# Kernel optimization log

Hardware: AMD Instinct MI355X
Metric: run time of the kernel (lower is better)

Reference implementation:

```python
import jax, jax.numpy as jnp
import numpy as np

V, T, E, HID = 50000, 32, 256, 512
H = HID // 2  # per-direction LSTM hidden
L, B = 512, 64


def setup_inputs() -> dict:
    key = jax.random.key(0)
    ks = jax.random.split(key, 18)
    p = lambda k, shape: (jax.random.normal(k, shape, jnp.float32) * 0.1)
    return {
        'seqs': jax.random.randint(ks[0], (L, B), 0, V),
        'tags': jax.random.randint(ks[1], (L, B), 0, T),
        'masks': jnp.ones((L, B), jnp.int32),
        'embed_table': p(ks[2], (V, E)),
        'W_ih_f': p(ks[3], (4 * H, E)), 'W_hh_f': p(ks[4], (4 * H, H)),
        'b_ih_f': p(ks[5], (4 * H,)),   'b_hh_f': p(ks[6], (4 * H,)),
        'W_ih_b': p(ks[7], (4 * H, E)), 'W_hh_b': p(ks[8], (4 * H, H)),
        'b_ih_b': p(ks[9], (4 * H,)),   'b_hh_b': p(ks[10], (4 * H,)),
        'W_out': p(ks[11], (T, HID)),   'b_out': p(ks[12], (T,)),
        'start_trans': p(ks[13], (T,)), 'end_trans': p(ks[14], (T,)),
        'trans': p(ks[15], (T, T)),
    }


def _lstm(xs, mask_b, W_ih, W_hh, b_ih, b_hh, reverse):
    # xs: [L,B,E], mask_b: [L,B] bool. Masked updates emulate packed sequences
    # (state frozen and output zeroed at padded steps).
    Bsz = xs.shape[1]
    Hd = W_hh.shape[1]
    x_proj = jnp.einsum('lbe,ge->lbg', xs, W_ih) + b_ih + b_hh  # precompute input gates

    def step(carry, inp):
        h, c = carry
        xg, m = inp
        gates = xg + h @ W_hh.T
        i, f, g, o = jnp.split(gates, 4, axis=-1)  # torch gate order i,f,g,o
        i, f, o = jax.nn.sigmoid(i), jax.nn.sigmoid(f), jax.nn.sigmoid(o)
        g = jnp.tanh(g)
        c_new = f * c + i * g
        h_new = o * jnp.tanh(c_new)
        m = m[:, None]
        h = jnp.where(m, h_new, h)
        c = jnp.where(m, c_new, c)
        out = jnp.where(m, h_new, 0.0)
        return (h, c), out

    init = (jnp.zeros((Bsz, Hd), xs.dtype), jnp.zeros((Bsz, Hd), xs.dtype))
    _, outs = jax.lax.scan(step, init, (x_proj, mask_b), reverse=reverse)
    return outs  # [L,B,H]


def reference(seqs, tags, masks, embed_table,
              W_ih_f, W_hh_f, b_ih_f, b_hh_f,
              W_ih_b, W_hh_b, b_ih_b, b_hh_b,
              W_out, b_out, start_trans, end_trans, trans):
    mb = masks.astype(bool)  # [L,B]
    emb = embed_table[seqs]  # [L,B,E]; dropout is identity in eval mode
    h_f = _lstm(emb, mb, W_ih_f, W_hh_f, b_ih_f, b_hh_f, reverse=False)
    h_b = _lstm(emb, mb, W_ih_b, W_hh_b, b_ih_b, b_hh_b, reverse=True)
    lstm_out = jnp.concatenate([h_f, h_b], axis=-1)           # [L,B,HID]
    emissions = jnp.einsum('lbh,th->lbt', lstm_out, W_out) + b_out  # [L,B,T]

    Lb, Bb = seqs.shape
    mf = masks[1:].astype(emissions.dtype)  # [L-1,B]

    # ---- gold path score (pytorch-crf numerator) ----
    e_scores = jnp.take_along_axis(emissions, tags[:, :, None], axis=2)[:, :, 0]  # [L,B]
    t_scores = trans[tags[:-1], tags[1:]]                                         # [L-1,B]
    lengths = masks.sum(0)
    last_tags = tags[lengths - 1, jnp.arange(Bb)]
    numerator = (start_trans[tags[0]] + e_scores[0]
                 + ((e_scores[1:] + t_scores) * mf).sum(0)
                 + end_trans[last_tags])  # [B]

    # ---- partition function (forward algorithm) ----
    def part_step(score, xs):
        e_t, m_t = xs  # [B,T], [B]
        nxt = jax.nn.logsumexp(score[:, :, None] + trans[None] + e_t[:, None, :], axis=1)
        return jnp.where(m_t[:, None], nxt, score), None

    score0 = start_trans[None, :] + emissions[0]
    score, _ = jax.lax.scan(part_step, score0, (emissions[1:], mb[1:]))
    log_z = jax.nn.logsumexp(score + end_trans[None, :], axis=1)  # [B]

    llh = numerator - log_z
    return -llh.mean()
```

## Files before the change

### kernel.cpp

```cpp
#include <hip/hip_runtime.h>
#include <hip/hip_bf16.h>
#include <stdint.h>

#define DEVINL __device__ __forceinline__

typedef __attribute__((ext_vector_type(8))) short short8;
typedef __attribute__((ext_vector_type(4))) float float4v;
typedef __attribute__((ext_vector_type(4))) int int4v;

#define NLC (-1.4426950408889634f)

DEVINL float uif(unsigned u) { union { unsigned u; float f; } v; v.u = u; return v.f; }
DEVINL float bf2f(short s) { return uif(((unsigned)(unsigned short)s) << 16); }
DEVINL unsigned short f2bf(float f) {
  union { float f; unsigned u; } v; v.f = f;
  unsigned r = v.u + 0x7FFFu + ((v.u >> 16) & 1u);
  return (unsigned short)(r >> 16);
}
DEVINL unsigned cvt_pk_bf16(float lo, float hi) {
  unsigned r;
  asm("v_cvt_pk_bf16_f32 %0, %1, %2" : "=v"(r) : "v"(lo), "v"(hi));
  return r;
}
DEVINL float ex2(float x) { return __builtin_amdgcn_exp2f(x); }
DEVINL float rcp_(float x) { return __builtin_amdgcn_rcpf(x); }
DEVINL void unp4(unsigned long long u, float* f) {
  unsigned lo = (unsigned)u, hi = (unsigned)(u >> 32);
  f[0] = uif(lo << 16); f[1] = uif(lo & 0xffff0000u);
  f[2] = uif(hi << 16); f[3] = uif(hi & 0xffff0000u);
}

#define LBAR() do { \
  asm volatile("s_waitcnt lgkmcnt(0)" ::: "memory"); \
  __builtin_amdgcn_sched_barrier(0); \
  __builtin_amdgcn_s_barrier(); \
  __builtin_amdgcn_sched_barrier(0); \
} while (0)

__global__ void k_cvt(const float* __restrict__ src, short* __restrict__ dst, int n8) {
  int i = blockIdx.x * blockDim.x + threadIdx.x;
  int stride = gridDim.x * blockDim.x;
  for (; i < n8; i += stride) {
    const float4v* s = (const float4v*)(src + (size_t)i * 8);
    float4v a = s[0], b = s[1];
    short8 o;
    o[0] = (short)f2bf(a[0]); o[1] = (short)f2bf(a[1]);
    o[2] = (short)f2bf(a[2]); o[3] = (short)f2bf(a[3]);
    o[4] = (short)f2bf(b[0]); o[5] = (short)f2bf(b[1]);
    o[6] = (short)f2bf(b[2]); o[7] = (short)f2bf(b[3]);
    ((short8*)dst)[i] = o;
  }
}

__global__ void k_bias(const float* __restrict__ a1, const float* __restrict__ a2,
                       const float* __restrict__ b1, const float* __restrict__ b2,
                       float* __restrict__ o) {
  int i = blockIdx.x * blockDim.x + threadIdx.x;
  o[i] = (i < 1024) ? (a1[i] + a2[i]) : (b1[i - 1024] + b2[i - 1024]);
}

__global__ void k_wmax(const float* __restrict__ Wf, const float* __restrict__ Wb,
                       unsigned* __restrict__ wmax) {
  int i = blockIdx.x * blockDim.x + threadIdx.x;
  int stride = gridDim.x * blockDim.x;
  unsigned mf = 0, mb = 0;
  for (int k = i; k < 262144; k += stride) {
    mf = max(mf, __float_as_uint(fabsf(Wf[k])));
    mb = max(mb, __float_as_uint(fabsf(Wb[k])));
  }
#pragma unroll
  for (int o = 32; o > 0; o >>= 1) {
    mf = max(mf, (unsigned)__shfl_down((int)mf, o));
    mb = max(mb, (unsigned)__shfl_down((int)mb, o));
  }
  if ((threadIdx.x & 63) == 0) { atomicMax(wmax + 0, mf); atomicMax(wmax + 1, mb); }
}

__global__ void k_wquant(const float* __restrict__ Wf, const float* __restrict__ Wb,
                         const float* __restrict__ wmax, char* __restrict__ whhQ) {
  int idx = blockIdx.x * blockDim.x + threadIdx.x;
  int dir = idx >> 16;
  int rem = idx & 65535;
  int r = rem >> 6;
  int k = (rem & 63) * 4;
  const float* W = dir ? Wb : Wf;
  float s = 127.0f / fmaxf(wmax[dir], 1e-20f);
  int g = r >> 8, unit = r & 255;
  int w = unit >> 6, m = (unit >> 4) & 3, row = unit & 15;
  int kt = k >> 6, l4 = (k >> 4) & 3, j = k & 15;
  int lane = l4 * 16 + row;
  unsigned out = 0;
#pragma unroll
  for (int t = 0; t < 4; ++t) {
    float v = W[(size_t)r * 256 + k + t] * s;
    int q = (int)rintf(v);
    q = q < -127 ? -127 : (q > 127 ? 127 : q);
    out |= ((unsigned)(q & 255)) << (8 * t);
  }
  *(unsigned*)(whhQ + (size_t)dir * 262144 + g * 65536 + w * 16384 + m * 4096 + kt * 1024 + lane * 16 + j) = out;
}

__launch_bounds__(256)
__global__ void k_xproj(const int* __restrict__ seqs, const short* __restrict__ embT,
                        const short* __restrict__ wihX, const float* __restrict__ biasX,
                        short* __restrict__ xproj) {
  __shared__ short As[128 * 256];
  __shared__ short Bs[128 * 256];
  __shared__ int ids[128];
  const int bm = blockIdx.x;
  const int tid = threadIdx.x;
  if (tid < 128) ids[tid] = seqs[bm * 128 + tid];
  __syncthreads();
#pragma unroll
  for (int i = 0; i < 16; ++i) {
    int task = tid + i * 256, row = task >> 5, kc = task & 31;
    short8 v = *(const short8*)(embT + (size_t)ids[row] * 256 + kc * 8);
    *(short8*)((char*)As + row * 512 + ((kc * 16) ^ ((row & 7) << 4))) = v;
  }
  __syncthreads();
  const int wave = tid >> 6, lane = tid & 63, l15 = lane & 15, l4 = lane >> 4;
  short8 af[2][8];
#pragma unroll
  for (int m = 0; m < 2; ++m) {
    int row = (wave * 2 + m) * 16 + l15;
#pragma unroll
    for (int kt = 0; kt < 8; ++kt)
      af[m][kt] = *(short8*)((char*)As + row * 512 + ((kt * 64 + l4 * 16) ^ ((row & 7) << 4)));
  }
#pragma unroll 1
  for (int bn = 0; bn < 16; ++bn) {
    __syncthreads();
#pragma unroll
    for (int i = 0; i < 16; ++i) {
      int task = tid + i * 256, row = task >> 5, kc = task & 31;
      short8 v = *(const short8*)(wihX + (size_t)(bn * 128 + row) * 256 + kc * 8);
      *(short8*)((char*)Bs + row * 512 + ((kc * 16) ^ ((row & 7) << 4))) = v;
    }
    __syncthreads();
    float4v acc[2][8];
#pragma unroll
    for (int m = 0; m < 2; ++m)
#pragma unroll
      for (int n = 0; n < 8; ++n) acc[m][n] = (float4v){0.f, 0.f, 0.f, 0.f};
#pragma unroll
    for (int kt = 0; kt < 8; ++kt) {
      const int kb = kt * 64 + l4 * 16;
      short8 b[8];
#pragma unroll
      for (int n = 0; n < 8; ++n) {
        int row = n * 16 + l15;
        b[n] = *(short8*)((char*)Bs + row * 512 + (kb ^ ((row & 7) << 4)));
      }
#pragma unroll
      for (int m = 0; m < 2; ++m)
#pragma unroll
        for (int n = 0; n < 8; ++n)
          acc[m][n] = __builtin_amdgcn_mfma_f32_16x16x32_bf16(af[m][kt], b[n], acc[m][n], 0, 0, 0);
    }
#pragma unroll
    for (int n = 0; n < 8; ++n) {
      int col = bn * 128 + n * 16 + l15;
      float bias = biasX[col];
      float scale = (((col >> 8) & 3) == 2) ? (2.f * NLC) : NLC;
#pragma unroll
      for (int m = 0; m < 2; ++m) {
        int token = bm * 128 + (wave * 2 + m) * 16 + l4 * 4;
#pragma unroll
        for (int q = 0; q < 4; ++q)
          xproj[(size_t)(token + q) * 2048 + col] = (short)f2bf((acc[m][n][q] + bias) * scale);
      }
    }
  }
}

__launch_bounds__(512, 2)
__global__ void k_lstm(const short* __restrict__ xproj, const char* __restrict__ whhQ,
                       const float* __restrict__ wmax, const int* __restrict__ mask_ws,
                       short* __restrict__ h_all) {
  __shared__ char lds_h[2][16 * 256];
  const int bid = blockIdx.x;
  const int dir = bid & 1, bq = bid >> 1;
  const int tid = threadIdx.x, w = tid >> 6, lane = tid & 63;
  const int beta = lane & 15, l4 = lane >> 4;
  const int bglob = bq * 16 + beta;
  const float wm = wmax[dir] * (1.0f / 16129.0f);
  const float facS = wm * NLC;
  const float facG = wm * 2.f * NLC;

  int4v wf[4][2][4];
  {
    const char* base = whhQ + (size_t)dir * 262144 + lane * 16;
#pragma unroll
    for (int g = 0; g < 4; ++g)
#pragma unroll
      for (int m = 0; m < 2; ++m) {
        int t = w * 2 + m;
#pragma unroll
        for (int kt = 0; kt < 4; ++kt)
          wf[g][m][kt] = *(const int4v*)(base + g * 65536 + (t >> 2) * 16384 + (t & 3) * 4096 + kt * 1024);
      }
  }

  int rd_off[4], wr_off[2];
#pragma unroll
  for (int kt = 0; kt < 4; ++kt)
    rd_off[kt] = beta * 256 + ((kt * 64 + l4 * 16) ^ ((beta & 7) << 4));
#pragma unroll
  for (int m = 0; m < 2; ++m)
    wr_off[m] = beta * 256 + ((w * 32 + m * 16 + l4 * 4) ^ ((beta & 7) << 4));

  if (tid < 256) ((int4v*)lds_h[0])[tid] = (int4v){0, 0, 0, 0};

  float c[2][4], hq[2][4];
#pragma unroll
  for (int m = 0; m < 2; ++m)
#pragma unroll
    for (int q = 0; q < 4; ++q) { c[m][q] = 0.f; hq[m][q] = 0.f; }

  const int t0 = dir ? 511 : 0;
  const int SD = dir ? -131072 : 131072;
  const int SM = dir ? -64 : 64;
  const int SH = dir ? -32768 : 32768;
  const short* px = xproj + (size_t)(t0 * 64 + bglob) * 2048 + dir * 1024 + w * 32 + l4 * 4;
  const int* pm = mask_ws + t0 * 64 + bglob;
  short* ph = h_all + (size_t)(t0 * 64 + bglob) * 512 + dir * 256 + w * 32 + l4 * 4;

  unsigned long long X0[4][2], X1[4][2];
  int m0, m1;
#pragma unroll
  for (int g = 0; g < 4; ++g)
#pragma unroll
    for (int m = 0; m < 2; ++m)
      X0[g][m] = *(const unsigned long long*)(px + g * 256 + m * 16);
  m0 = *pm;
  px += SD; pm += SM;

  auto SUB = [&](unsigned long long (&xc)[4][2], int& mc,
                 unsigned long long (&xn)[4][2], int& mn,
                 const char* rb, char* wb) {
    LBAR();
    int4v bfr[4];
#pragma unroll
    for (int kt = 0; kt < 4; ++kt) bfr[kt] = *(const int4v*)(rb + rd_off[kt]);

#pragma unroll
    for (int g = 0; g < 4; ++g)
#pragma unroll
      for (int m = 0; m < 2; ++m)
        xn[g][m] = *(const unsigned long long*)(px + g * 256 + m * 16);
    mn = *pm;
    px += SD; pm += SM;

    int4v iacc[4][2];
#pragma unroll
    for (int g = 0; g < 4; ++g)
#pragma unroll
      for (int m = 0; m < 2; ++m) {
        int4v t = __builtin_amdgcn_mfma_i32_16x16x64_i8(wf[g][m][0], bfr[0], (int4v){0, 0, 0, 0}, 0, 0, 0);
        t = __builtin_amdgcn_mfma_i32_16x16x64_i8(wf[g][m][1], bfr[1], t, 0, 0, 0);
        t = __builtin_amdgcn_mfma_i32_16x16x64_i8(wf[g][m][2], bfr[2], t, 0, 0, 0);
        iacc[g][m] = __builtin_amdgcn_mfma_i32_16x16x64_i8(wf[g][m][3], bfr[3], t, 0, 0, 0);
      }

#pragma unroll
    for (int m = 0; m < 2; ++m) {
      float xi[4], xf[4], xg[4], xo[4];
      unp4(xc[0][m], xi); unp4(xc[1][m], xf); unp4(xc[2][m], xg); unp4(xc[3][m], xo);
      unsigned qb[4]; float ov[4];
#pragma unroll
      for (int q = 0; q < 4; ++q) {
        float ai = fmaf((float)iacc[0][m][q], facS, xi[q]);
        float af_ = fmaf((float)iacc[1][m][q], facS, xf[q]);
        float ag = fmaf((float)iacc[2][m][q], facG, xg[q]);
        float ao = fmaf((float)iacc[3][m][q], facS, xo[q]);
        float Ei = fminf(ex2(ai), 1e30f);
        float Ef = fminf(ex2(af_), 1e30f);
        float Eg = fminf(ex2(ag), 1e30f);
        float Eo = fminf(ex2(ao), 1e30f);
        float ig = (1.f - Eg) * rcp_((1.f + Ei) * (1.f + Eg));
        float fv = rcp_(1.f + Ef);
        float cn = fmaf(fv, c[m][q], ig);
        float Ec = fminf(ex2(cn * (2.f * NLC)), 1e30f);
        float hn = (1.f - Ec) * rcp_((1.f + Eo) * (1.f + Ec));
        c[m][q] = mc ? cn : c[m][q];
        float hv = mc ? hn : hq[m][q];
        hq[m][q] = hv;
        ov[q] = mc ? hn : 0.f;
        qb[q] = __float_as_uint(fmaf(hv, 127.f, 12582912.f));
      }
      unsigned p0 = __builtin_amdgcn_perm(qb[1], qb[0], 0x0c0c0400u);
      unsigned p1 = __builtin_amdgcn_perm(qb[3], qb[2], 0x0c0c0400u);
      unsigned qpack = __builtin_amdgcn_perm(p1, p0, 0x05040100u);
      *(unsigned*)(wb + wr_off[m]) = qpack;
      uint2 ob;
      ob.x = cvt_pk_bf16(ov[0], ov[1]);
      ob.y = cvt_pk_bf16(ov[2], ov[3]);
      *(uint2*)(ph + m * 16) = ob;
    }
    ph += SH;
  };

#pragma unroll 1
  for (int s2 = 0; s2 < 256; ++s2) {
    SUB(X0, m0, X1, m1, lds_h[0], lds_h[1]);
    SUB(X1, m1, X0, m0, lds_h[1], lds_h[0]);
  }
}

__launch_bounds__(256)
__global__ void k_emis(const short* __restrict__ h_all, const short* __restrict__ woutX,
                       const float* __restrict__ bout, float* __restrict__ emis) {
  const int tid = threadIdx.x, wave = tid >> 6, lane = tid & 63;
  const int l15 = lane & 15, l4 = lane >> 4;
  const int token0 = blockIdx.x * 256 + wave * 64;
  float4v acc[4][2];
#pragma unroll
  for (int m = 0; m < 4; ++m)
#pragma unroll
    for (int n = 0; n < 2; ++n) acc[m][n] = (float4v){0.f, 0.f, 0.f, 0.f};
#pragma unroll
  for (int kt = 0; kt < 16; ++kt) {
    short8 b[2];
#pragma unroll
    for (int n = 0; n < 2; ++n)
      b[n] = *(const short8*)(woutX + (size_t)(n * 16 + l15) * 512 + kt * 32 + l4 * 8);
#pragma unroll
    for (int m = 0; m < 4; ++m) {
      short8 a = *(const short8*)(h_all + (size_t)(token0 + m * 16 + l15) * 512 + kt * 32 + l4 * 8);
#pragma unroll
      for (int n = 0; n < 2; ++n)
        acc[m][n] = __builtin_amdgcn_mfma_f32_16x16x32_bf16(a, b[n], acc[m][n], 0, 0, 0);
    }
  }
#pragma unroll
  for (int n = 0; n < 2; ++n) {
    float bias = bout[n * 16 + l15];
#pragma unroll
    for (int m = 0; m < 4; ++m) {
      int token = token0 + m * 16 + l4 * 4;
#pragma unroll
      for (int q = 0; q < 4; ++q)
        emis[(size_t)(token + q) * 32 + n * 16 + l15] = acc[m][n][q] + bias;
    }
  }
}

__launch_bounds__(64)
__global__ void k_crf(const float* __restrict__ emis, const int* __restrict__ tags,
                      const int* __restrict__ masks, const float* __restrict__ strans,
                      const float* __restrict__ etrans, const float* __restrict__ trans,
                      float* __restrict__ out) {
  __shared__ float trans_s[1024];
  __shared__ float score_s[32];
  const float L2E = 1.4426950408889634f;
  const int b = blockIdx.x, lane = threadIdx.x;
  for (int i = lane; i < 1024; i += 64) trans_s[i] = trans[i];

  float num = 0.f; int lensum = 0;
#pragma unroll 1
  for (int i = 0; i < 8; ++i) {
    int t = lane + i * 64;
    int tg = tags[t * 64 + b];
    int m = masks[t * 64 + b];
    lensum += m;
    float e = emis[(size_t)(t * 64 + b) * 32 + tg];
    if (t == 0) num += strans[tg] + e;
    else if (m) num += e + trans[tags[(t - 1) * 64 + b] * 32 + tg];
  }
#pragma unroll
  for (int o = 32; o > 0; o >>= 1) { num += __shfl_down(num, o); lensum += __shfl_down(lensum, o); }
  num = __shfl(num, 0);
  lensum = __shfl(lensum, 0);
  num += etrans[tags[(lensum - 1) * 64 + b]];
  __syncthreads();

  const int jp = lane & 31, half = lane >> 5;
  if (lane < 32) score_s[jp] = strans[jp] + emis[(size_t)b * 32 + jp];
  __syncthreads();

  float e_next = emis[(size_t)(64 + b) * 32 + jp];
#pragma unroll 1
  for (int t = 1; t < 512; ++t) {
    float e = e_next;
    if (t < 511) e_next = emis[(size_t)((t + 1) * 64 + b) * 32 + jp];
    int m = masks[t * 64 + b];
    float v[16], mx = -1e30f;
#pragma unroll
    for (int j = 0; j < 16; ++j) {
      v[j] = score_s[half * 16 + j] + trans_s[(half * 16 + j) * 32 + jp];
      mx = fmaxf(mx, v[j]);
    }
    float sum = 0.f;
#pragma unroll
    for (int j = 0; j < 16; ++j) sum += ex2((v[j] - mx) * L2E);
    float mo = __shfl_xor(mx, 32), so = __shfl_xor(sum, 32);
    float mn2 = fmaxf(mx, mo);
    sum = sum * ex2((mx - mn2) * L2E) + so * ex2((mo - mn2) * L2E);
    float nxt = e + mn2 + __builtin_amdgcn_logf(sum) * (1.f / L2E);
    float cur = score_s[jp];
    float ns = m ? nxt : cur;
    __syncthreads();
    if (lane < 32) score_s[jp] = ns;
    __syncthreads();
  }

  float vv = (lane < 32) ? (score_s[jp] + etrans[jp]) : -1e30f;
  float mx = vv;
#pragma unroll
  for (int o = 32; o > 0; o >>= 1) mx = fmaxf(mx, __shfl_xor(mx, o));
  float sm = (lane < 32) ? ex2((vv - mx) * L2E) : 0.f;
#pragma unroll
  for (int o = 32; o > 0; o >>= 1) sm += __shfl_xor(sm, o);
  float lz = mx + __builtin_amdgcn_logf(sm) * (1.f / L2E);
  if (lane == 0) atomicAdd(out, -(num - lz) * (1.0f / 64.0f));
}

extern "C" void kernel_launch(void* const* d_in, const int* in_sizes, int n_in,
                              void* d_out, int out_size, void* d_ws, size_t ws_size,
                              hipStream_t stream) {
  const int*   seqs  = (const int*)d_in[0];
  const int*   tags  = (const int*)d_in[1];
  const int*   masks = (const int*)d_in[2];
  const float* embed = (const float*)d_in[3];
  const float* Wihf  = (const float*)d_in[4];
  const float* Whhf  = (const float*)d_in[5];
  const float* bihf  = (const float*)d_in[6];
  const float* bhhf  = (const float*)d_in[7];
  const float* Wihb  = (const float*)d_in[8];
  const float* Whhb  = (const float*)d_in[9];
  const float* bihb  = (const float*)d_in[10];
  const float* bhhb  = (const float*)d_in[11];
  const float* Wout  = (const float*)d_in[12];
  const float* bout  = (const float*)d_in[13];
  const float* strn  = (const float*)d_in[14];
  const float* etrn  = (const float*)d_in[15];
  const float* trn   = (const float*)d_in[16];
  float* outf = (float*)d_out;

  char* ws = (char*)d_ws;
  short* xproj = (short*)(ws + 262144);
  short* h_all = (short*)(ws + 134479872);
  float* emis  = (float*)(ws + 168034304);
  short* embT  = (short*)(ws + 172228608);
  short* wihX  = (short*)(ws + 197828608);
  char*  whhQ  = (char*)(ws + 198877184);
  short* woutX = (short*)(ws + 199401472);
  float* biasX = (float*)(ws + 199434240);
  unsigned* wmaxb = (unsigned*)(ws + 199442432);
  int* mask_ws = (int*)(ws + 199442944);

  hipMemsetAsync(d_out, 0, 4, stream);
  hipMemsetAsync(wmaxb, 0, 8, stream);
  hipMemcpyAsync(mask_ws, masks, 131072, hipMemcpyDeviceToDevice, stream);

  k_cvt<<<2048, 256, 0, stream>>>(embed, embT, 1600000);
  k_cvt<<<128, 256, 0, stream>>>(Wihf, wihX, 32768);
  k_cvt<<<128, 256, 0, stream>>>(Wihb, wihX + 262144, 32768);
  k_cvt<<<8, 256, 0, stream>>>(Wout, woutX, 2048);
  k_bias<<<2, 1024, 0, stream>>>(bihf, bhhf, bihb, bhhb, biasX);
  k_wmax<<<64, 256, 0, stream>>>(Whhf, Whhb, wmaxb);
  k_wquant<<<512, 256, 0, stream>>>(Whhf, Whhb, (const float*)wmaxb, whhQ);
  k_xproj<<<256, 256, 0, stream>>>(seqs, embT, wihX, biasX, xproj);
  k_lstm<<<8, 512, 0, stream>>>(xproj, whhQ, (const float*)wmaxb, mask_ws, h_all);
  k_emis<<<128, 256, 0, stream>>>(h_all, woutX, bout, emis);
  k_crf<<<64, 64, 0, stream>>>(emis, tags, masks, strn, etrn, trn, outf);
}
```

Before: 1.590 ms.

## Split LSTM recurrence across 16 waves per block, one hidden tile each

The recurrent LSTM kernel now launches 1024 threads per block, so each of 16 waves owns a single 16-column hidden tile instead of two. Per-wave weight registers, MFMA chains and gate math are halved, which shortens the serial per-timestep critical path. The gate math also drops the clamps on three exponentials and folds the (1+a)(1+b) products into FMAs. In exchange, the per-step LDS barrier now synchronises twice as many waves, and the unclamped exponentials rely on the reciprocal behaving well at infinity.

```diff
diff --git a/kernel.cpp b/kernel.cpp
--- a/kernel.cpp
+++ b/kernel.cpp
@@ -173,7 +173,7 @@
   }
 }
 
-__launch_bounds__(512, 2)
+__launch_bounds__(1024, 1)
 __global__ void k_lstm(const short* __restrict__ xproj, const char* __restrict__ whhQ,
                        const float* __restrict__ wmax, const int* __restrict__ mask_ws,
                        short* __restrict__ h_all) {
@@ -187,56 +187,46 @@
   const float facS = wm * NLC;
   const float facG = wm * 2.f * NLC;
 
-  int4v wf[4][2][4];
+  int4v wf[4][4];
   {
-    const char* base = whhQ + (size_t)dir * 262144 + lane * 16;
+    const char* base = whhQ + (size_t)dir * 262144 + (w >> 2) * 16384 + (w & 3) * 4096 + lane * 16;
 #pragma unroll
     for (int g = 0; g < 4; ++g)
 #pragma unroll
-      for (int m = 0; m < 2; ++m) {
-        int t = w * 2 + m;
-#pragma unroll
-        for (int kt = 0; kt < 4; ++kt)
-          wf[g][m][kt] = *(const int4v*)(base + g * 65536 + (t >> 2) * 16384 + (t & 3) * 4096 + kt * 1024);
-      }
-  }
-
-  int rd_off[4], wr_off[2];
+      for (int kt = 0; kt < 4; ++kt)
+        wf[g][kt] = *(const int4v*)(base + g * 65536 + kt * 1024);
+  }
+
+  int rd_off[4];
 #pragma unroll
   for (int kt = 0; kt < 4; ++kt)
     rd_off[kt] = beta * 256 + ((kt * 64 + l4 * 16) ^ ((beta & 7) << 4));
-#pragma unroll
-  for (int m = 0; m < 2; ++m)
-    wr_off[m] = beta * 256 + ((w * 32 + m * 16 + l4 * 4) ^ ((beta & 7) << 4));
+  const int wr_off = beta * 256 + ((w * 16 + l4 * 4) ^ ((beta & 7) << 4));
 
   if (tid < 256) ((int4v*)lds_h[0])[tid] = (int4v){0, 0, 0, 0};
 
-  float c[2][4], hq[2][4];
-#pragma unroll
-  for (int m = 0; m < 2; ++m)
-#pragma unroll
-    for (int q = 0; q < 4; ++q) { c[m][q] = 0.f; hq[m][q] = 0.f; }
+  float c[4], hq[4];
+#pragma unroll
+  for (int q = 0; q < 4; ++q) { c[q] = 0.f; hq[q] = 0.f; }
 
   const int t0 = dir ? 511 : 0;
   const int SD = dir ? -131072 : 131072;
   const int SM = dir ? -64 : 64;
   const int SH = dir ? -32768 : 32768;
-  const short* px = xproj + (size_t)(t0 * 64 + bglob) * 2048 + dir * 1024 + w * 32 + l4 * 4;
+  const short* px = xproj + (size_t)(t0 * 64 + bglob) * 2048 + dir * 1024 + w * 16 + l4 * 4;
   const int* pm = mask_ws + t0 * 64 + bglob;
-  short* ph = h_all + (size_t)(t0 * 64 + bglob) * 512 + dir * 256 + w * 32 + l4 * 4;
-
-  unsigned long long X0[4][2], X1[4][2];
+  short* ph = h_all + (size_t)(t0 * 64 + bglob) * 512 + dir * 256 + w * 16 + l4 * 4;
+
+  unsigned long long X0[4], X1[4];
   int m0, m1;
 #pragma unroll
   for (int g = 0; g < 4; ++g)
-#pragma unroll
-    for (int m = 0; m < 2; ++m)
-      X0[g][m] = *(const unsigned long long*)(px + g * 256 + m * 16);
+    X0[g] = *(const unsigned long long*)(px + g * 256);
   m0 = *pm;
   px += SD; pm += SM;
 
-  auto SUB = [&](unsigned long long (&xc)[4][2], int& mc,
-                 unsigned long long (&xn)[4][2], int& mn,
+  auto SUB = [&](unsigned long long (&xc)[4], int& mc,
+                 unsigned long long (&xn)[4], int& mn,
                  const char* rb, char* wb) {
     LBAR();
     int4v bfr[4];
@@ -245,58 +235,53 @@
 
 #pragma unroll
     for (int g = 0; g < 4; ++g)
-#pragma unroll
-      for (int m = 0; m < 2; ++m)
-        xn[g][m] = *(const unsigned long long*)(px + g * 256 + m * 16);
+      xn[g] = *(const unsigned long long*)(px + g * 256);
     mn = *pm;
     px += SD; pm += SM;
 
-    int4v iacc[4][2];
-#pragma unroll
-    for (int g = 0; g < 4; ++g)
-#pragma unroll
-      for (int m = 0; m < 2; ++m) {
-        int4v t = __builtin_amdgcn_mfma_i32_16x16x64_i8(wf[g][m][0], bfr[0], (int4v){0, 0, 0, 0}, 0, 0, 0);
-        t = __builtin_amdgcn_mfma_i32_16x16x64_i8(wf[g][m][1], bfr[1], t, 0, 0, 0);
-        t = __builtin_amdgcn_mfma_i32_16x16x64_i8(wf[g][m][2], bfr[2], t, 0, 0, 0);
-        iacc[g][m] = __builtin_amdgcn_mfma_i32_16x16x64_i8(wf[g][m][3], bfr[3], t, 0, 0, 0);
-      }
-
-#pragma unroll
-    for (int m = 0; m < 2; ++m) {
-      float xi[4], xf[4], xg[4], xo[4];
-      unp4(xc[0][m], xi); unp4(xc[1][m], xf); unp4(xc[2][m], xg); unp4(xc[3][m], xo);
-      unsigned qb[4]; float ov[4];
-#pragma unroll
-      for (int q = 0; q < 4; ++q) {
-        float ai = fmaf((float)iacc[0][m][q], facS, xi[q]);
-        float af_ = fmaf((float)iacc[1][m][q], facS, xf[q]);
-        float ag = fmaf((float)iacc[2][m][q], facG, xg[q]);
-        float ao = fmaf((float)iacc[3][m][q], facS, xo[q]);
-        float Ei = fminf(ex2(ai), 1e30f);
-        float Ef = fminf(ex2(af_), 1e30f);
-        float Eg = fminf(ex2(ag), 1e30f);
-        float Eo = fminf(ex2(ao), 1e30f);
-        float ig = (1.f - Eg) * rcp_((1.f + Ei) * (1.f + Eg));
-        float fv = rcp_(1.f + Ef);
-        float cn = fmaf(fv, c[m][q], ig);
-        float Ec = fminf(ex2(cn * (2.f * NLC)), 1e30f);
-        float hn = (1.f - Ec) * rcp_((1.f + Eo) * (1.f + Ec));
-        c[m][q] = mc ? cn : c[m][q];
-        float hv = mc ? hn : hq[m][q];
-        hq[m][q] = hv;
-        ov[q] = mc ? hn : 0.f;
-        qb[q] = __float_as_uint(fmaf(hv, 127.f, 12582912.f));
-      }
-      unsigned p0 = __builtin_amdgcn_perm(qb[1], qb[0], 0x0c0c0400u);
-      unsigned p1 = __builtin_amdgcn_perm(qb[3], qb[2], 0x0c0c0400u);
-      unsigned qpack = __builtin_amdgcn_perm(p1, p0, 0x05040100u);
-      *(unsigned*)(wb + wr_off[m]) = qpack;
-      uint2 ob;
-      ob.x = cvt_pk_bf16(ov[0], ov[1]);
-      ob.y = cvt_pk_bf16(ov[2], ov[3]);
-      *(uint2*)(ph + m * 16) = ob;
-    }
+    int4v iacc[4];
+#pragma unroll
+    for (int g = 0; g < 4; ++g) {
+      int4v t = __builtin_amdgcn_mfma_i32_16x16x64_i8(wf[g][0], bfr[0], (int4v){0, 0, 0, 0}, 0, 0, 0);
+      t = __builtin_amdgcn_mfma_i32_16x16x64_i8(wf[g][1], bfr[1], t, 0, 0, 0);
+      t = __builtin_amdgcn_mfma_i32_16x16x64_i8(wf[g][2], bfr[2], t, 0, 0, 0);
+      iacc[g] = __builtin_amdgcn_mfma_i32_16x16x64_i8(wf[g][3], bfr[3], t, 0, 0, 0);
+    }
+
+    float xi[4], xf[4], xg[4], xo[4];
+    unp4(xc[0], xi); unp4(xc[1], xf); unp4(xc[2], xg); unp4(xc[3], xo);
+    unsigned qb[4]; float ov[4];
+#pragma unroll
+    for (int q = 0; q < 4; ++q) {
+      float ai = fmaf((float)iacc[0][q], facS, xi[q]);
+      float af_ = fmaf((float)iacc[1][q], facS, xf[q]);
+      float ag = fmaf((float)iacc[2][q], facG, xg[q]);
+      float ao = fmaf((float)iacc[3][q], facS, xo[q]);
+      float Ei = ex2(ai);
+      float Ef = ex2(af_);
+      float Eg = fminf(ex2(ag), 1e30f);
+      float Eo = ex2(ao);
+      float t1 = 1.f + Ei;
+      float ig = (1.f - Eg) * rcp_(fmaf(t1, Eg, t1));
+      float fv = rcp_(1.f + Ef);
+      float cn = fmaf(fv, c[q], ig);
+      float Ec = fminf(ex2(cn * (2.f * NLC)), 1e30f);
+      float t2 = 1.f + Eo;
+      float hn = (1.f - Ec) * rcp_(fmaf(t2, Ec, t2));
+      c[q] = mc ? cn : c[q];
+      float hv = mc ? hn : hq[q];
+      hq[q] = hv;
+      ov[q] = mc ? hn : 0.f;
+      qb[q] = __float_as_uint(fmaf(hv, 127.f, 12582912.f));
+    }
+    unsigned p0 = __builtin_amdgcn_perm(qb[1], qb[0], 0x0c0c0400u);
+    unsigned p1 = __builtin_amdgcn_perm(qb[3], qb[2], 0x0c0c0400u);
+    unsigned qpack = __builtin_amdgcn_perm(p1, p0, 0x05040100u);
+    *(unsigned*)(wb + wr_off) = qpack;
+    uint2 ob;
+    ob.x = cvt_pk_bf16(ov[0], ov[1]);
+    ob.y = cvt_pk_bf16(ov[2], ov[3]);
+    *(uint2*)ph = ob;
     ph += SH;
   };
 
@@ -461,7 +446,7 @@
   k_wmax<<<64, 256, 0, stream>>>(Whhf, Whhb, wmaxb);
   k_wquant<<<512, 256, 0, stream>>>(Whhf, Whhb, (const float*)wmaxb, whhQ);
   k_xproj<<<256, 256, 0, stream>>>(seqs, embT, wihX, biasX, xproj);
-  k_lstm<<<8, 512, 0, stream>>>(xproj, whhQ, (const float*)wmaxb, mask_ws, h_all);
+  k_lstm<<<8, 1024, 0, stream>>>(xproj, whhQ, (const float*)wmaxb, mask_ws, h_all);
   k_emis<<<128, 256, 0, stream>>>(h_all, woutX, bout, emis);
   k_crf<<<64, 64, 0, stream>>>(emis, tags, masks, strn, etrn, trn, outf);
 }
```

Result: slower. 1.806 ms (+13.6%).
